# Performance work log

Measured on AMD Instinct MI355X. Metric: run time of the kernel, lower is better.

## Reference

```python
import jax, jax.numpy as jnp
import numpy as np

H = 256
NUM_HEADS = 4
HEAD_DIM = H // NUM_HEADS


def _mlp(x, W1, b1, W2, b2):
    # Linear(2H->H) + ReLU + (dropout=identity in eval) + Linear(H->H)
    h = jax.nn.relu(x @ W1.T + b1)
    return h @ W2.T + b2


def setup_inputs() -> dict:
    key = jax.random.key(0)
    ks = jax.random.split(key, 24)
    s2h = 1.0 / np.sqrt(2 * H)
    sh = 1.0 / np.sqrt(H)
    inp = {
        'qubit_embeddings': jax.random.normal(ks[0], (65536, H), jnp.float32),
        'qpu_embeddings': jax.random.normal(ks[1], (64, H), jnp.float32),
        'gate_embeddings': jax.random.normal(ks[2], (65536, H), jnp.float32),
        'all_embeddings': jax.random.normal(ks[3], (131072, H), jnp.float32),
        'time_table': jax.random.normal(ks[4], (1000, H), jnp.float32),
        'map_W1': jax.random.normal(ks[5], (H, 2 * H), jnp.float32) * s2h,
        'map_b1': jnp.zeros((H,), jnp.float32),
        'map_W2': jax.random.normal(ks[6], (H, H), jnp.float32) * sh,
        'map_b2': jnp.zeros((H,), jnp.float32),
        'sch_W1': jax.random.normal(ks[7], (H, 2 * H), jnp.float32) * s2h,
        'sch_b1': jnp.zeros((H,), jnp.float32),
        'sch_W2': jax.random.normal(ks[8], (H, H), jnp.float32) * sh,
        'sch_b2': jnp.zeros((H,), jnp.float32),
        'qg_W1': jax.random.normal(ks[9], (H, H), jnp.float32) * sh,
        'qg_b1': jnp.zeros((H,), jnp.float32),
        'qg_W2': jax.random.normal(ks[10], (H, H), jnp.float32) * sh,
        'qg_b2': jnp.zeros((H,), jnp.float32),
        'attn_Wq': jax.random.normal(ks[11], (H, H), jnp.float32) * sh,
        'attn_bq': jnp.zeros((H,), jnp.float32),
        'attn_Wk': jax.random.normal(ks[12], (H, H), jnp.float32) * sh,
        'attn_bk': jnp.zeros((H,), jnp.float32),
        'attn_Wv': jax.random.normal(ks[13], (H, H), jnp.float32) * sh,
        'attn_bv': jnp.zeros((H,), jnp.float32),
        'attn_Wo': jax.random.normal(ks[14], (H, H), jnp.float32) * sh,
        'attn_bo': jnp.zeros((H,), jnp.float32),
        'map_qubit': jax.random.randint(ks[15], (131072,), 0, 65536, jnp.int32),
        'map_qpu': jax.random.randint(ks[16], (131072,), 0, 64, jnp.int32),
        'sched_gate': jax.random.randint(ks[17], (131072,), 0, 65536, jnp.int32),
        'sched_time': jax.random.randint(ks[18], (131072,), 0, 1000, jnp.int32),
    }
    return inp


def reference(qubit_embeddings, qpu_embeddings, gate_embeddings, all_embeddings,
              time_table, map_W1, map_b1, map_W2, map_b2,
              sch_W1, sch_b1, sch_W2, sch_b2,
              qg_W1, qg_b1, qg_W2, qg_b2,
              attn_Wq, attn_bq, attn_Wk, attn_bk, attn_Wv, attn_bv,
              attn_Wo, attn_bo,
              map_qubit, map_qpu, sched_gate, sched_time):
    # Vectorized form of the per-action Python loop: gather + concat + MLP.
    map_in = jnp.concatenate([qubit_embeddings[map_qubit], qpu_embeddings[map_qpu]], axis=-1)  # [Nm, 2H]
    map_keys = _mlp(map_in, map_W1, map_b1, map_W2, map_b2)                                    # [Nm, H]
    sch_in = jnp.concatenate([gate_embeddings[sched_gate], time_table[sched_time]], axis=-1)   # [Ns, 2H]
    sch_keys = _mlp(sch_in, sch_W1, sch_b1, sch_W2, sch_b2)                                    # [Ns, H]
    keys = jnp.concatenate([map_keys, sch_keys], axis=0)                                       # [A, H]

    g = all_embeddings.mean(axis=0)                                                            # [H]
    query = jax.nn.relu(g @ qg_W1.T + qg_b1) @ qg_W2.T + qg_b2                                 # [H]

    # MultiheadAttention: batch=1, q_len=1, kv_len=A (dropout=0 in eval, mask all-valid).
    q = (query @ attn_Wq.T + attn_bq).reshape(NUM_HEADS, HEAD_DIM)
    k = (keys @ attn_Wk.T + attn_bk).reshape(-1, NUM_HEADS, HEAD_DIM)
    v = (keys @ attn_Wv.T + attn_bv).reshape(-1, NUM_HEADS, HEAD_DIM)
    scores = jnp.einsum('hd,ahd->ha', q, k) / jnp.sqrt(jnp.asarray(HEAD_DIM, q.dtype))
    w = jax.nn.softmax(scores, axis=-1)                                                        # [heads, A]
    ctx = jnp.einsum('ha,ahd->hd', w, v).reshape(H)
    attn_out = ctx @ attn_Wo.T + attn_bo                                                       # [H]

    action_logits = keys @ attn_out                                                            # [A]
    action_probs = jax.nn.softmax(action_logits, axis=-1)
    return action_probs, action_logits
```

## Files before the change

kernel.cpp:

```cpp
#include <hip/hip_runtime.h>
#include <cstdint>
#include <cstddef>

typedef __bf16 bf16_t;
typedef __bf16 bf16x8 __attribute__((ext_vector_type(8)));
typedef __bf16 bf16x4 __attribute__((ext_vector_type(4)));
typedef float f32x4 __attribute__((ext_vector_type(4)));

#define A_TOTAL 262144
#define NMAP    131072

__global__ __launch_bounds__(256) void k_w1b16(
    const float* __restrict__ mW1, const float* __restrict__ sW1,
    bf16_t* __restrict__ dst) {
  int e = blockIdx.x * 256 + threadIdx.x;
  int slice = e >> 16, idx = e & 65535;
  int n = idx >> 8, k = idx & 255;
  float v;
  switch (slice) {
    case 0:  v = mW1[n * 512 + k]; break;
    case 1:  v = mW1[n * 512 + 256 + k]; break;
    case 2:  v = sW1[n * 512 + k]; break;
    default: v = sW1[n * 512 + 256 + k]; break;
  }
  dst[e] = (bf16_t)v;
}

__global__ __launch_bounds__(256) void k_mean(const float* __restrict__ A,
                                              float* __restrict__ part) {
  int t = threadIdx.x, b = blockIdx.x;
  const float* base = A + (size_t)b * 512 * 256 + t;
  float s = 0.f;
  for (int r = 0; r < 512; ++r) s += base[(size_t)r * 256];
  part[b * 256 + t] = s;
}

__global__ __launch_bounds__(256) void k_front(
    const float* __restrict__ meanPart,
    const float* __restrict__ qgW1, const float* __restrict__ qgb1,
    const float* __restrict__ qgW2, const float* __restrict__ qgb2,
    const float* __restrict__ Wq,  const float* __restrict__ bq,
    const float* __restrict__ Wk,
    const float* __restrict__ mW2, const float* __restrict__ sW2,
    float* __restrict__ qw) {
  __shared__ float g[256], h1[256], qry[256], qv[256];
  __shared__ float qks[4][256];
  int t = threadIdx.x;
  float s = 0.f;
  for (int b = 0; b < 256; ++b) s += meanPart[b * 256 + t];
  g[t] = s * (1.0f / 131072.0f);
  __syncthreads();
  {
    const f32x4* row = (const f32x4*)(qgW1 + (size_t)t * 256);
    float acc = 0.f;
    for (int k = 0; k < 64; ++k) {
      f32x4 w = row[k];
      acc += w[0] * g[4 * k] + w[1] * g[4 * k + 1] + w[2] * g[4 * k + 2] + w[3] * g[4 * k + 3];
    }
    h1[t] = fmaxf(acc + qgb1[t], 0.f);
  }
  __syncthreads();
  {
    const f32x4* row = (const f32x4*)(qgW2 + (size_t)t * 256);
    float acc = 0.f;
    for (int k = 0; k < 64; ++k) {
      f32x4 w = row[k];
      acc += w[0] * h1[4 * k] + w[1] * h1[4 * k + 1] + w[2] * h1[4 * k + 2] + w[3] * h1[4 * k + 3];
    }
    qry[t] = acc + qgb2[t];
  }
  __syncthreads();
  {
    const f32x4* row = (const f32x4*)(Wq + (size_t)t * 256);
    float acc = 0.f;
    for (int k = 0; k < 64; ++k) {
      f32x4 w = row[k];
      acc += w[0] * qry[4 * k] + w[1] * qry[4 * k + 1] + w[2] * qry[4 * k + 2] + w[3] * qry[4 * k + 3];
    }
    qv[t] = acc + bq[t];
  }
  __syncthreads();
  for (int h = 0; h < 4; ++h) {
    float acc = 0.f;
    for (int d = 0; d < 64; ++d) acc += qv[h * 64 + d] * Wk[(size_t)(h * 64 + d) * 256 + t];
    qks[h][t] = acc * 0.125f;
  }
  __syncthreads();
  for (int tab = 0; tab < 2; ++tab) {
    const float* W2 = tab ? sW2 : mW2;
    float acc0 = 0.f, acc1 = 0.f, acc2 = 0.f, acc3 = 0.f;
    for (int n = 0; n < 256; ++n) {
      float wv = W2[(size_t)n * 256 + t];
      acc0 += qks[0][n] * wv;
      acc1 += qks[1][n] * wv;
      acc2 += qks[2][n] * wv;
      acc3 += qks[3][n] * wv;
    }
    float* dst = qw + tab * 1024;
    dst[0 * 256 + t] = acc0;
    dst[1 * 256 + t] = acc1;
    dst[2 * 256 + t] = acc2;
    dst[3 * 256 + t] = acc3;
  }
}

__global__ __launch_bounds__(512, 4) void gemm_direct3(
    const float* __restrict__ A0, int M0, const bf16_t* __restrict__ W0,
    const float* __restrict__ b0, bf16_t* __restrict__ C0, int split,
    const float* __restrict__ A1, int M1, const bf16_t* __restrict__ W1,
    const float* __restrict__ b1, bf16_t* __restrict__ C1) {
  __shared__ __align__(16) bf16_t Xo[128][264];
  int blk = blockIdx.x;
  const float* A; int M; const bf16_t* W; const float* bias; bf16_t* C; int bid;
  if (blk < split) { A = A0; M = M0; W = W0; bias = b0; C = C0; bid = blk; }
  else             { A = A1; M = M1; W = W1; bias = b1; C = C1; bid = blk - split; }
  int t = threadIdx.x;
  int w = t >> 6, lane = t & 63;
  int lm = lane & 15, q = lane >> 4;
  int mloc0 = (w & 1) * 64;
  int m0 = bid * 128 + mloc0;
  int c0 = (w >> 1) * 64;
  int rows[4];
#pragma unroll
  for (int i = 0; i < 4; ++i) {
    int m = m0 + i * 16 + lm;
    rows[i] = m < M ? m : M - 1;
  }
  f32x4 acc[4][4] = {};
#pragma unroll
  for (int kt = 0; kt < 8; ++kt) {
    int k0 = kt * 32 + q * 8;
    bf16x8 b[4];
#pragma unroll
    for (int j = 0; j < 4; ++j)
      b[j] = *(const bf16x8*)(W + (size_t)(c0 + j * 16 + lm) * 256 + k0);
#pragma unroll
    for (int i = 0; i < 4; ++i) {
      const float* src = A + (size_t)rows[i] * 256 + k0;
      f32x4 lo = *(const f32x4*)src;
      f32x4 hi = *(const f32x4*)(src + 4);
      bf16x8 a;
#pragma unroll
      for (int x = 0; x < 4; ++x) { a[x] = (bf16_t)lo[x]; a[x + 4] = (bf16_t)hi[x]; }
#pragma unroll
      for (int j = 0; j < 4; ++j)
        acc[i][j] = __builtin_amdgcn_mfma_f32_16x16x32_bf16(a, b[j], acc[i][j], 0, 0, 0);
    }
  }
#pragma unroll
  for (int j = 0; j < 4; ++j) {
    int col = c0 + j * 16 + lm;
    float bb = bias ? bias[col] : 0.f;
#pragma unroll
    for (int i = 0; i < 4; ++i)
#pragma unroll
      for (int r = 0; r < 4; ++r)
        Xo[mloc0 + i * 16 + q * 4 + r][col] = (bf16_t)(acc[i][j][r] + bb);
  }
  __syncthreads();
  size_t tile0 = (size_t)bid * 128;
  const char* lds = (const char*)&Xo[0][0];
#pragma unroll
  for (int s = 0; s < 8; ++s) {
    int flat = s * 8192 + t * 16;
    int row = flat >> 9, colb = flat & 511;
    if (tile0 + (size_t)row < (size_t)M) {
      uint4 v = *(const uint4*)(lds + row * 528 + colb);
      *(uint4*)((char*)C + tile0 * 512 + (size_t)flat) = v;
    }
  }
}

__global__ __launch_bounds__(256) void k_gx(
    const bf16_t* __restrict__ Pa0, const bf16_t* __restrict__ Pb0,
    const int* __restrict__ idxA0, const int* __restrict__ idxB0,
    const bf16_t* __restrict__ Pa1, const bf16_t* __restrict__ Pb1,
    const int* __restrict__ idxA1, const int* __restrict__ idxB1,
    const float* __restrict__ qw,
    bf16_t* __restrict__ X, float* __restrict__ scores,
    float* __restrict__ partMax) {
  __shared__ float qs[4][256];
  __shared__ float sc[4][64];
  int t = threadIdx.x;
  int b = blockIdx.x;
  int rows0 = b * 64;
  int half = rows0 >= NMAP ? 1 : 0;
  const bf16_t* Pa = half ? Pa1 : Pa0;
  const bf16_t* Pb = half ? Pb1 : Pb0;
  const int* idxA = half ? idxA1 : idxA0;
  const int* idxB = half ? idxB1 : idxB0;
  int lrow0 = rows0 - half * NMAP;

  {
    f32x4 v = *(const f32x4*)(qw + half * 1024 + t * 4);
    *(f32x4*)&((float*)qs)[t * 4] = v;
  }

  int rg = t >> 5;
  int cl = t & 31;
  int ia[8], ib[8];
#pragma unroll
  for (int it = 0; it < 8; ++it) {
    ia[it] = idxA[lrow0 + it * 8 + rg];
    ib[it] = idxB[lrow0 + it * 8 + rg];
  }
  __syncthreads();

#pragma unroll
  for (int it = 0; it < 8; ++it) {
    int rowg = it * 8 + rg;
    bf16x8 a8 = *(const bf16x8*)(Pa + (size_t)ia[it] * 256 + cl * 8);
    bf16x8 b8 = *(const bf16x8*)(Pb + (size_t)ib[it] * 256 + cl * 8);
    float x[8];
    bf16x8 xo;
#pragma unroll
    for (int e = 0; e < 8; ++e) {
      x[e] = fmaxf((float)a8[e] + (float)b8[e], 0.f);
      xo[e] = (bf16_t)x[e];
    }
    *(bf16x8*)(X + (size_t)(rows0 + rowg) * 256 + cl * 8) = xo;
    float p[4] = {0.f, 0.f, 0.f, 0.f};
#pragma unroll
    for (int h = 0; h < 4; ++h)
#pragma unroll
      for (int e = 0; e < 8; ++e)
        p[h] += x[e] * qs[h][cl * 8 + e];
#pragma unroll
    for (int h = 0; h < 4; ++h) {
#pragma unroll
      for (int o = 16; o > 0; o >>= 1) p[h] += __shfl_xor(p[h], o);
      if (cl == 0) sc[h][rowg] = p[h];
    }
  }
  __syncthreads();
  {
    int h = t >> 6, l = t & 63;
    float v = sc[h][l];
    scores[(size_t)h * A_TOTAL + rows0 + l] = v;
    float m = v;
#pragma unroll
    for (int o = 32; o > 0; o >>= 1) m = fmaxf(m, __shfl_xor(m, o));
    if (l == 0) partMax[h * 4096 + b] = m;
  }
}

__global__ __launch_bounds__(256) void k_smax2(const float* __restrict__ pM,
                                               float* __restrict__ Mh) {
  int t = threadIdx.x;
  __shared__ float red[256];
  for (int h = 0; h < 4; ++h) {
    float m = -3.4e38f;
    for (int i = t; i < 4096; i += 256) m = fmaxf(m, pM[h * 4096 + i]);
    red[t] = m;
    __syncthreads();
    for (int s = 128; s > 0; s >>= 1) {
      if (t < s) red[t] = fmaxf(red[t], red[t + s]);
      __syncthreads();
    }
    if (t == 0) Mh[h] = red[0];
    __syncthreads();
  }
}

__global__ __launch_bounds__(256) void k_ssum(const float* __restrict__ scores,
                                              const float* __restrict__ Mh,
                                              float* __restrict__ part) {
  int b = blockIdx.x, t = threadIdx.x;
  float m = Mh[b >> 6];
  const float* base = scores + (size_t)b * 4096;
  float s = 0.f;
  for (int i = 0; i < 16; ++i) s += __expf(base[i * 256 + t] - m);
  __shared__ float red[256];
  red[t] = s;
  __syncthreads();
  for (int st = 128; st > 0; st >>= 1) {
    if (t < st) red[t] += red[t + st];
    __syncthreads();
  }
  if (t == 0) part[b] = red[0];
}

__global__ __launch_bounds__(256) void k_ssum2(const float* __restrict__ part,
                                               float* __restrict__ invS) {
  int t = threadIdx.x;
  __shared__ float red[256];
  red[t] = part[t];
  __syncthreads();
  for (int s = 32; s > 0; s >>= 1) {
    if ((t & 63) < s) red[t] += red[t + s];
    __syncthreads();
  }
  if ((t & 63) == 0) invS[t >> 6] = 1.0f / red[t];
}

__global__ __launch_bounds__(256) void k_u3(
    const bf16_t* __restrict__ X, const float* __restrict__ scores,
    const float* __restrict__ Mh, const float* __restrict__ invS,
    float* __restrict__ y, float* __restrict__ shalf) {
  __shared__ float wl[4][512];
  __shared__ float uloc[8][4][256];
  int t = threadIdx.x;
  int a0 = blockIdx.x * 512;
  int half = blockIdx.x >> 8;
#pragma unroll
  for (int i = 0; i < 8; ++i) {
    int e = i * 256 + t;
    int h = e >> 9, rr = e & 511;
    wl[h][rr] = __expf(scores[(size_t)h * A_TOTAL + a0 + rr] - Mh[h]) * invS[h];
  }
  __syncthreads();
  {
    int h = t >> 6, l = t & 63;
    float s = 0.f;
#pragma unroll
    for (int j = 0; j < 8; ++j) s += wl[h][l + j * 64];
#pragma unroll
    for (int o = 32; o > 0; o >>= 1) s += __shfl_xor(s, o);
    if (l == 0) atomicAdd(&shalf[half * 4 + h], s);
  }
  int tc = t & 31, rh = t >> 5;
  float acc[4][8] = {};
  for (int rr = 0; rr < 64; ++rr) {
    int al = rh * 64 + rr;
    bf16x8 kv = *(const bf16x8*)(X + (size_t)(a0 + al) * 256 + tc * 8);
    float f[8];
#pragma unroll
    for (int e = 0; e < 8; ++e) f[e] = (float)kv[e];
#pragma unroll
    for (int h = 0; h < 4; ++h) {
      float wv = wl[h][al];
#pragma unroll
      for (int e = 0; e < 8; ++e) acc[h][e] += wv * f[e];
    }
  }
#pragma unroll
  for (int h = 0; h < 4; ++h)
#pragma unroll
    for (int e = 0; e < 8; ++e) uloc[rh][h][tc * 8 + e] = acc[h][e];
  __syncthreads();
#pragma unroll
  for (int h = 0; h < 4; ++h) {
    float v = 0.f;
#pragma unroll
    for (int g = 0; g < 8; ++g) v += uloc[g][h][t];
    atomicAdd(&y[(half * 4 + h) * 256 + t], v);
  }
}

__global__ __launch_bounds__(256) void k_attn2(
    const float* __restrict__ y,
    const float* __restrict__ shalf,
    const float* __restrict__ mW2, const float* __restrict__ sW2,
    const float* __restrict__ mb2, const float* __restrict__ sb2,
    const float* __restrict__ Wv, const float* __restrict__ bv,
    const float* __restrict__ Wo, const float* __restrict__ bo,
    float* __restrict__ attnv, float* __restrict__ c01) {
  __shared__ float ys[2][4][256];
  __shared__ float us[4][256];
  __shared__ float ctx[256];
  __shared__ float att[256];
  __shared__ float r0[4], r1[4];
  int t = threadIdx.x;
#pragma unroll
  for (int i = 0; i < 8; ++i) ((float*)ys)[i * 256 + t] = y[i * 256 + t];
  __syncthreads();
  {
    int j = t;
    float a0 = 0.f, a1 = 0.f, a2 = 0.f, a3 = 0.f;
    const f32x4* rm = (const f32x4*)(mW2 + (size_t)j * 256);
    const f32x4* rs = (const f32x4*)(sW2 + (size_t)j * 256);
    for (int k = 0; k < 64; ++k) {
      f32x4 wm = rm[k], wsv = rs[k];
#pragma unroll
      for (int e = 0; e < 4; ++e) {
        float w0 = wm[e], w1 = wsv[e];
        int kk = k * 4 + e;
        a0 += ys[0][0][kk] * w0 + ys[1][0][kk] * w1;
        a1 += ys[0][1][kk] * w0 + ys[1][1][kk] * w1;
        a2 += ys[0][2][kk] * w0 + ys[1][2][kk] * w1;
        a3 += ys[0][3][kk] * w0 + ys[1][3][kk] * w1;
      }
    }
    float bm = mb2[j], bs = sb2[j];
    us[0][j] = a0 + shalf[0] * bm + shalf[4] * bs;
    us[1][j] = a1 + shalf[1] * bm + shalf[5] * bs;
    us[2][j] = a2 + shalf[2] * bm + shalf[6] * bs;
    us[3][j] = a3 + shalf[3] * bm + shalf[7] * bs;
  }
  __syncthreads();
  {
    int h = t >> 6;
    const f32x4* row = (const f32x4*)(Wv + (size_t)t * 256);
    const f32x4* uh = (const f32x4*)us[h];
    float acc = 0.f;
    for (int k = 0; k < 64; ++k) {
      f32x4 w = row[k], x = uh[k];
      acc += w[0] * x[0] + w[1] * x[1] + w[2] * x[2] + w[3] * x[3];
    }
    ctx[t] = acc + bv[t];
  }
  __syncthreads();
  {
    const f32x4* row = (const f32x4*)(Wo + (size_t)t * 256);
    const f32x4* cx = (const f32x4*)ctx;
    float acc = 0.f;
    for (int k = 0; k < 64; ++k) {
      f32x4 w = row[k], x = cx[k];
      acc += w[0] * x[0] + w[1] * x[1] + w[2] * x[2] + w[3] * x[3];
    }
    float v = acc + bo[t];
    att[t] = v;
    attnv[t] = v;
  }
  __syncthreads();
  {
    float p0 = mb2[t] * att[t], p1 = sb2[t] * att[t];
#pragma unroll
    for (int o = 32; o > 0; o >>= 1) {
      p0 += __shfl_xor(p0, o);
      p1 += __shfl_xor(p1, o);
    }
    if ((t & 63) == 0) { r0[t >> 6] = p0; r1[t >> 6] = p1; }
    __syncthreads();
    if (t == 0) c01[0] = r0[0] + r0[1] + r0[2] + r0[3];
    if (t == 1) c01[1] = r1[0] + r1[1] + r1[2] + r1[3];
  }
}

__global__ __launch_bounds__(256) void k_zc(
    const float* __restrict__ mW2, const float* __restrict__ sW2,
    const float* __restrict__ attnv, bf16_t* __restrict__ zpad) {
  int tab = blockIdx.x, t = threadIdx.x;
  const float* W2 = tab ? sW2 : mW2;
  __shared__ float att[256];
  att[t] = attnv[t];
  __syncthreads();
  float acc = 0.f;
  for (int j = 0; j < 256; ++j) acc += W2[(size_t)j * 256 + t] * att[j];
  bf16_t* dst = zpad + (size_t)tab * 16 * 256;
  dst[t] = (bf16_t)acc;
#pragma unroll
  for (int i = 1; i < 16; ++i) dst[i * 256 + t] = (bf16_t)0.f;
}

__global__ __launch_bounds__(256) void k_logits3(
    const bf16_t* __restrict__ X, const bf16_t* __restrict__ zpad,
    const float* __restrict__ c01,
    float* __restrict__ out_logits, float* __restrict__ blockMax) {
  int t = threadIdx.x;
  int w = t >> 6, lane = t & 63;
  int lm = lane & 15, q = lane >> 4;
  int half = blockIdx.x >> 9;
  float c = c01[half];
  int m0 = blockIdx.x * 256 + w * 64;
  const bf16_t* zp = zpad + (size_t)half * 16 * 256;
  bf16x8 b[8];
#pragma unroll
  for (int kt = 0; kt < 8; ++kt)
    b[kt] = *(const bf16x8*)(zp + lm * 256 + kt * 32 + q * 8);
  f32x4 acc[4] = {};
#pragma unroll
  for (int i = 0; i < 4; ++i) {
    const bf16_t* arow = X + (size_t)(m0 + i * 16 + lm) * 256 + q * 8;
#pragma unroll
    for (int kt = 0; kt < 8; ++kt) {
      bf16x8 a = *(const bf16x8*)(arow + kt * 32);
      acc[i] = __builtin_amdgcn_mfma_f32_16x16x32_bf16(a, b[kt], acc[i], 0, 0, 0);
    }
  }
  float lmax = -3.4e38f;
  if (lm == 0) {
#pragma unroll
    for (int i = 0; i < 4; ++i) {
      f32x4 v4;
#pragma unroll
      for (int rr = 0; rr < 4; ++rr) {
        float v = acc[i][rr] + c;
        v4[rr] = v;
        lmax = fmaxf(lmax, v);
      }
      *(f32x4*)(out_logits + m0 + i * 16 + q * 4) = v4;
    }
  }
  float m1 = fmaxf(lmax, __shfl_xor(lmax, 16));
  float m2 = fmaxf(m1, __shfl_xor(m1, 32));
  __shared__ float red[4];
  if (lane == 0) red[w] = m2;
  __syncthreads();
  if (t == 0)
    blockMax[blockIdx.x] = fmaxf(fmaxf(red[0], red[1]), fmaxf(red[2], red[3]));
}

__global__ __launch_bounds__(256) void k_lred1(const float* __restrict__ bm,
                                               float* __restrict__ Ml) {
  int t = threadIdx.x;
  float m = -3.4e38f;
  for (int i = t; i < 1024; i += 256) m = fmaxf(m, bm[i]);
  __shared__ float red[256];
  red[t] = m;
  __syncthreads();
  for (int s = 128; s > 0; s >>= 1) {
    if (t < s) red[t] = fmaxf(red[t], red[t + s]);
    __syncthreads();
  }
  if (t == 0) Ml[0] = red[0];
}

__global__ __launch_bounds__(256) void k_lsum(const float* __restrict__ logits,
                                              const float* __restrict__ Ml,
                                              float* __restrict__ part) {
  int t = threadIdx.x, b = blockIdx.x;
  float m = Ml[0];
  float s = __expf(logits[b * 512 + t] - m) + __expf(logits[b * 512 + 256 + t] - m);
  __shared__ float red[256];
  red[t] = s;
  __syncthreads();
  for (int st = 128; st > 0; st >>= 1) {
    if (t < st) red[t] += red[t + st];
    __syncthreads();
  }
  if (t == 0) part[b] = red[0];
}

__global__ __launch_bounds__(256) void k_lred2(const float* __restrict__ part,
                                               float* __restrict__ invSl) {
  int t = threadIdx.x;
  float s = part[t] + part[t + 256];
  __shared__ float red[256];
  red[t] = s;
  __syncthreads();
  for (int st = 128; st > 0; st >>= 1) {
    if (t < st) red[t] += red[t + st];
    __syncthreads();
  }
  if (t == 0) invSl[0] = 1.0f / red[0];
}

__global__ __launch_bounds__(256) void k_probs(const float* __restrict__ logits,
                                               const float* __restrict__ Ml,
                                               const float* __restrict__ invSl,
                                               float* __restrict__ probs) {
  int i = blockIdx.x * 256 + threadIdx.x;
  probs[i] = __expf(logits[i] - Ml[0]) * invSl[0];
}

extern "C" void kernel_launch(void* const* d_in, const int* in_sizes, int n_in,
                              void* d_out, int out_size, void* d_ws, size_t ws_size,
                              hipStream_t stream) {
  const float* qubit_emb = (const float*)d_in[0];
  const float* qpu_emb   = (const float*)d_in[1];
  const float* gate_emb  = (const float*)d_in[2];
  const float* all_emb   = (const float*)d_in[3];
  const float* time_tab  = (const float*)d_in[4];
  const float* map_W1 = (const float*)d_in[5];
  const float* map_b1 = (const float*)d_in[6];
  const float* map_W2 = (const float*)d_in[7];
  const float* map_b2 = (const float*)d_in[8];
  const float* sch_W1 = (const float*)d_in[9];
  const float* sch_b1 = (const float*)d_in[10];
  const float* sch_W2 = (const float*)d_in[11];
  const float* sch_b2 = (const float*)d_in[12];
  const float* qg_W1 = (const float*)d_in[13];
  const float* qg_b1 = (const float*)d_in[14];
  const float* qg_W2 = (const float*)d_in[15];
  const float* qg_b2 = (const float*)d_in[16];
  const float* Wq = (const float*)d_in[17];
  const float* bq = (const float*)d_in[18];
  const float* Wk = (const float*)d_in[19];
  const float* Wv = (const float*)d_in[21];
  const float* bv = (const float*)d_in[22];
  const float* Wo = (const float*)d_in[23];
  const float* bo = (const float*)d_in[24];
  const int* map_qubit  = (const int*)d_in[25];
  const int* map_qpu    = (const int*)d_in[26];
  const int* sched_gate = (const int*)d_in[27];
  const int* sched_time = (const int*)d_in[28];
  (void)in_sizes; (void)n_in; (void)out_size;

  char* ws = (char*)d_ws;
  size_t off = 0;
  auto alloc = [&](size_t b) { size_t r = off; off += (b + 255) & ~(size_t)255; return r; };
  size_t XB    = alloc((size_t)A_TOTAL * 256 * 2);
  size_t PQ    = alloc((size_t)65536 * 256 * 2);
  size_t PG    = alloc((size_t)65536 * 256 * 2);
  size_t PP    = alloc((size_t)128 * 256 * 2);
  size_t PT    = alloc((size_t)1024 * 256 * 2);
  size_t W1B   = alloc((size_t)4 * 65536 * 2);
  size_t QW    = alloc((size_t)2 * 4 * 256 * 4);
  size_t SCORE = alloc((size_t)4 * A_TOTAL * 4);
  size_t MPART = alloc((size_t)256 * 256 * 4);
  size_t ZPAD  = alloc((size_t)2 * 16 * 256 * 2);
  size_t ATTNV = alloc(256 * 4);
  size_t Y     = alloc(2 * 4 * 256 * 4);
  size_t SH    = alloc(2 * 4 * 4);
  size_t C01   = alloc(2 * 4);
  size_t PMAX  = alloc(4 * 4096 * 4);
  size_t MH    = alloc(4 * 4);
  size_t SINV  = alloc(4 * 4);
  size_t BMAX  = alloc(1024 * 4);
  size_t ML    = alloc(4);
  size_t SLINV = alloc(4);
  size_t LPART = alloc(512 * 4);
  size_t SPART = alloc(256 * 4);
  if (off > ws_size) return;

  bf16_t* xP     = (bf16_t*)(ws + XB);
  bf16_t* pqP    = (bf16_t*)(ws + PQ);
  bf16_t* pgP    = (bf16_t*)(ws + PG);
  bf16_t* ppP    = (bf16_t*)(ws + PP);
  bf16_t* ptP    = (bf16_t*)(ws + PT);
  bf16_t* w1bP   = (bf16_t*)(ws + W1B);
  float*  qwP    = (float*)(ws + QW);
  float*  scoreP = (float*)(ws + SCORE);
  float*  mpartP = (float*)(ws + MPART);
  bf16_t* zpadP  = (bf16_t*)(ws + ZPAD);
  float*  attnvP = (float*)(ws + ATTNV);
  float*  yP     = (float*)(ws + Y);
  float*  shP    = (float*)(ws + SH);
  float*  c01P   = (float*)(ws + C01);
  float*  pmaxP  = (float*)(ws + PMAX);
  float*  mhP    = (float*)(ws + MH);
  float*  sinvP  = (float*)(ws + SINV);
  float*  bmaxP  = (float*)(ws + BMAX);
  float*  mlP    = (float*)(ws + ML);
  float*  slinvP = (float*)(ws + SLINV);
  float*  lpartP = (float*)(ws + LPART);
  float*  spartP = (float*)(ws + SPART);

  float* probsOut  = (float*)d_out;
  float* logitsOut = probsOut + A_TOTAL;

  hipMemsetAsync(yP, 0, 8448, stream);

  k_w1b16<<<1024, 256, 0, stream>>>(map_W1, sch_W1, w1bP);
  k_mean<<<256, 256, 0, stream>>>(all_emb, mpartP);
  k_front<<<1, 256, 0, stream>>>(mpartP, qg_W1, qg_b1, qg_W2, qg_b2,
                                 Wq, bq, Wk, map_W2, sch_W2, qwP);

  gemm_direct3<<<1024, 512, 0, stream>>>(
      qubit_emb, 65536, w1bP + 0 * 65536, nullptr, pqP, 512,
      gate_emb,  65536, w1bP + 2 * 65536, nullptr, pgP);
  gemm_direct3<<<9, 512, 0, stream>>>(
      qpu_emb, 64,   w1bP + 1 * 65536, map_b1, ppP, 1,
      time_tab, 1000, w1bP + 3 * 65536, sch_b1, ptP);

  k_gx<<<4096, 256, 0, stream>>>(
      pqP, ppP, map_qubit, map_qpu,
      pgP, ptP, sched_gate, sched_time,
      qwP, xP, scoreP, pmaxP);

  k_smax2<<<1, 256, 0, stream>>>(pmaxP, mhP);
  k_ssum<<<256, 256, 0, stream>>>(scoreP, mhP, spartP);
  k_ssum2<<<1, 256, 0, stream>>>(spartP, sinvP);

  k_u3<<<512, 256, 0, stream>>>(xP, scoreP, mhP, sinvP, yP, shP);
  k_attn2<<<1, 256, 0, stream>>>(yP, shP, map_W2, sch_W2, map_b2, sch_b2,
                                 Wv, bv, Wo, bo, attnvP, c01P);
  k_zc<<<2, 256, 0, stream>>>(map_W2, sch_W2, attnvP, zpadP);

  k_logits3<<<1024, 256, 0, stream>>>(xP, zpadP, c01P, logitsOut, bmaxP);
  k_lred1<<<1, 256, 0, stream>>>(bmaxP, mlP);
  k_lsum<<<512, 256, 0, stream>>>(logitsOut, mlP, lpartP);
  k_lred2<<<1, 256, 0, stream>>>(lpartP, slinvP);
  k_probs<<<1024, 256, 0, stream>>>(logitsOut, mlP, slinvP, probsOut);
}
```

Before: 717.1 us.

## Fuse softmax reductions via last-block pattern and parallelize tail matvecs

Online max/sum partials are now computed inside k_gx and k_logits4. A last-block atomic counter does the final reduction there, which removes several small reduction kernels and one re-read of the scores and logits arrays. The single-block attention tail (k_attn2, k_zc) is split into multi-block matvec kernels, and c01 is accumulated with atomics. k_mean is vectorised to f32x4 loads, and the GEMM epilogue LDS buffer is halved to allow higher occupancy. The memset is extended to cover the counters and c01, and atomic float accumulation changes summation order.

Result: slower. 1.597 ms (+122.7%).

```diff
diff --git a/kernel.cpp b/kernel.cpp
--- a/kernel.cpp
+++ b/kernel.cpp
@@ -28,11 +28,20 @@
 
 __global__ __launch_bounds__(256) void k_mean(const float* __restrict__ A,
                                               float* __restrict__ part) {
+  __shared__ f32x4 sred[4][64];
   int t = threadIdx.x, b = blockIdx.x;
-  const float* base = A + (size_t)b * 512 * 256 + t;
-  float s = 0.f;
-  for (int r = 0; r < 512; ++r) s += base[(size_t)r * 256];
-  part[b * 256 + t] = s;
+  int cg = t & 63, rs = t >> 6;
+  const float* base = A + ((size_t)b * 512 + rs * 128) * 256 + cg * 4;
+  f32x4 acc = {};
+#pragma unroll 4
+  for (int r = 0; r < 128; ++r)
+    acc += *(const f32x4*)(base + (size_t)r * 256);
+  sred[rs][cg] = acc;
+  __syncthreads();
+  if (t < 64) {
+    f32x4 tot = sred[0][t] + sred[1][t] + sred[2][t] + sred[3][t];
+    *(f32x4*)(part + b * 256 + t * 4) = tot;
+  }
 }
 
 __global__ __launch_bounds__(256) void k_front(
@@ -104,12 +113,12 @@
   }
 }
 
-__global__ __launch_bounds__(512, 4) void gemm_direct3(
+__global__ __launch_bounds__(512, 8) void gemm_direct4(
     const float* __restrict__ A0, int M0, const bf16_t* __restrict__ W0,
     const float* __restrict__ b0, bf16_t* __restrict__ C0, int split,
     const float* __restrict__ A1, int M1, const bf16_t* __restrict__ W1,
     const float* __restrict__ b1, bf16_t* __restrict__ C1) {
-  __shared__ __align__(16) bf16_t Xo[128][264];
+  __shared__ __align__(16) bf16_t Xo[64][264];
   int blk = blockIdx.x;
   const float* A; int M; const bf16_t* W; const float* bias; bf16_t* C; int bid;
   if (blk < split) { A = A0; M = M0; W = W0; bias = b0; C = C0; bid = blk; }
@@ -117,8 +126,7 @@
   int t = threadIdx.x;
   int w = t >> 6, lane = t & 63;
   int lm = lane & 15, q = lane >> 4;
-  int mloc0 = (w & 1) * 64;
-  int m0 = bid * 128 + mloc0;
+  int m0 = bid * 128 + (w & 1) * 64;
   int c0 = (w >> 1) * 64;
   int rows[4];
 #pragma unroll
@@ -148,25 +156,31 @@
     }
   }
 #pragma unroll
-  for (int j = 0; j < 4; ++j) {
-    int col = c0 + j * 16 + lm;
-    float bb = bias ? bias[col] : 0.f;
-#pragma unroll
-    for (int i = 0; i < 4; ++i)
-#pragma unroll
-      for (int r = 0; r < 4; ++r)
-        Xo[mloc0 + i * 16 + q * 4 + r][col] = (bf16_t)(acc[i][j][r] + bb);
-  }
-  __syncthreads();
-  size_t tile0 = (size_t)bid * 128;
-  const char* lds = (const char*)&Xo[0][0];
-#pragma unroll
-  for (int s = 0; s < 8; ++s) {
-    int flat = s * 8192 + t * 16;
-    int row = flat >> 9, colb = flat & 511;
-    if (tile0 + (size_t)row < (size_t)M) {
-      uint4 v = *(const uint4*)(lds + row * 528 + colb);
-      *(uint4*)((char*)C + tile0 * 512 + (size_t)flat) = v;
+  for (int p = 0; p < 2; ++p) {
+    if (p) __syncthreads();
+    if ((w & 1) == p) {
+#pragma unroll
+      for (int j = 0; j < 4; ++j) {
+        int col = c0 + j * 16 + lm;
+        float bb = bias ? bias[col] : 0.f;
+#pragma unroll
+        for (int i = 0; i < 4; ++i)
+#pragma unroll
+          for (int r = 0; r < 4; ++r)
+            Xo[i * 16 + q * 4 + r][col] = (bf16_t)(acc[i][j][r] + bb);
+      }
+    }
+    __syncthreads();
+    size_t tile0 = (size_t)bid * 128 + p * 64;
+    const char* lds = (const char*)&Xo[0][0];
+#pragma unroll
+    for (int s = 0; s < 4; ++s) {
+      int flat = s * 8192 + t * 16;
+      int row = flat >> 9, colb = flat & 511;
+      if (tile0 + (size_t)row < (size_t)M) {
+        uint4 v = *(const uint4*)(lds + row * 528 + colb);
+        *(uint4*)((char*)C + tile0 * 512 + (size_t)flat) = v;
+      }
     }
   }
 }
@@ -178,9 +192,12 @@
     const int* __restrict__ idxA1, const int* __restrict__ idxB1,
     const float* __restrict__ qw,
     bf16_t* __restrict__ X, float* __restrict__ scores,
-    float* __restrict__ partMax) {
+    float* __restrict__ partMax, float* __restrict__ partSum,
+    int* __restrict__ cnt, float* __restrict__ Mh, float* __restrict__ sinv) {
   __shared__ float qs[4][256];
   __shared__ float sc[4][64];
+  __shared__ float redM[256], redS[256];
+  __shared__ int isLast;
   int t = threadIdx.x;
   int b = blockIdx.x;
   int rows0 = b * 64;
@@ -240,57 +257,42 @@
     float m = v;
 #pragma unroll
     for (int o = 32; o > 0; o >>= 1) m = fmaxf(m, __shfl_xor(m, o));
-    if (l == 0) partMax[h * 4096 + b] = m;
-  }
-}
-
-__global__ __launch_bounds__(256) void k_smax2(const float* __restrict__ pM,
-                                               float* __restrict__ Mh) {
-  int t = threadIdx.x;
-  __shared__ float red[256];
+    float s = __expf(v - m);
+#pragma unroll
+    for (int o = 32; o > 0; o >>= 1) s += __shfl_xor(s, o);
+    if (l == 0) {
+      partMax[h * 4096 + b] = m;
+      partSum[h * 4096 + b] = s;
+    }
+  }
+  __threadfence();
+  __syncthreads();
+  if (t == 0) isLast = (atomicAdd(cnt, 1) == (int)gridDim.x - 1);
+  __syncthreads();
+  if (!isLast) return;
+  __threadfence();
   for (int h = 0; h < 4; ++h) {
-    float m = -3.4e38f;
-    for (int i = t; i < 4096; i += 256) m = fmaxf(m, pM[h * 4096 + i]);
-    red[t] = m;
+    float m = -3.4e38f, s = 0.f;
+    for (int i = t; i < 4096; i += 256) {
+      float pm = partMax[h * 4096 + i], ps = partSum[h * 4096 + i];
+      float nm = fmaxf(m, pm);
+      s = s * __expf(m - nm) + ps * __expf(pm - nm);
+      m = nm;
+    }
+    redM[t] = m; redS[t] = s;
     __syncthreads();
-    for (int s = 128; s > 0; s >>= 1) {
-      if (t < s) red[t] = fmaxf(red[t], red[t + s]);
+    for (int st = 128; st > 0; st >>= 1) {
+      if (t < st) {
+        float m2 = redM[t + st], s2 = redS[t + st];
+        float nm = fmaxf(redM[t], m2);
+        redS[t] = redS[t] * __expf(redM[t] - nm) + s2 * __expf(m2 - nm);
+        redM[t] = nm;
+      }
       __syncthreads();
     }
-    if (t == 0) Mh[h] = red[0];
+    if (t == 0) { Mh[h] = redM[0]; sinv[h] = 1.0f / redS[0]; }
     __syncthreads();
   }
-}
-
-__global__ __launch_bounds__(256) void k_ssum(const float* __restrict__ scores,
-                                              const float* __restrict__ Mh,
-                                              float* __restrict__ part) {
-  int b = blockIdx.x, t = threadIdx.x;
-  float m = Mh[b >> 6];
-  const float* base = scores + (size_t)b * 4096;
-  float s = 0.f;
-  for (int i = 0; i < 16; ++i) s += __expf(base[i * 256 + t] - m);
-  __shared__ float red[256];
-  red[t] = s;
-  __syncthreads();
-  for (int st = 128; st > 0; st >>= 1) {
-    if (t < st) red[t] += red[t + st];
-    __syncthreads();
-  }
-  if (t == 0) part[b] = red[0];
-}
-
-__global__ __launch_bounds__(256) void k_ssum2(const float* __restrict__ part,
-                                               float* __restrict__ invS) {
-  int t = threadIdx.x;
-  __shared__ float red[256];
-  red[t] = part[t];
-  __syncthreads();
-  for (int s = 32; s > 0; s >>= 1) {
-    if ((t & 63) < s) red[t] += red[t + s];
-    __syncthreads();
-  }
-  if ((t & 63) == 0) invS[t >> 6] = 1.0f / red[t];
 }
 
 __global__ __launch_bounds__(256) void k_u3(
@@ -347,106 +349,110 @@
   }
 }
 
-__global__ __launch_bounds__(256) void k_attn2(
-    const float* __restrict__ y,
-    const float* __restrict__ shalf,
+__global__ __launch_bounds__(256) void k_u4(
+    const float* __restrict__ y, const float* __restrict__ shalf,
     const float* __restrict__ mW2, const float* __restrict__ sW2,
     const float* __restrict__ mb2, const float* __restrict__ sb2,
-    const float* __restrict__ Wv, const float* __restrict__ bv,
-    const float* __restrict__ Wo, const float* __restrict__ bo,
-    float* __restrict__ attnv, float* __restrict__ c01) {
-  __shared__ float ys[2][4][256];
-  __shared__ float us[4][256];
-  __shared__ float ctx[256];
-  __shared__ float att[256];
-  __shared__ float r0[4], r1[4];
+    float* __restrict__ u) {
+  __shared__ float wsum[4][4];
+  int j = blockIdx.x, t = threadIdx.x;
+  int w = t >> 6, lane = t & 63;
+  float pm = mW2[(size_t)j * 256 + t], ps = sW2[(size_t)j * 256 + t];
+  float p[4];
+#pragma unroll
+  for (int h = 0; h < 4; ++h)
+    p[h] = y[(0 + h) * 256 + t] * pm + y[(4 + h) * 256 + t] * ps;
+#pragma unroll
+  for (int h = 0; h < 4; ++h)
+#pragma unroll
+    for (int o = 32; o > 0; o >>= 1) p[h] += __shfl_xor(p[h], o);
+  if (lane == 0)
+#pragma unroll
+    for (int h = 0; h < 4; ++h) wsum[w][h] = p[h];
+  __syncthreads();
+  if (t < 4) {
+    float tot = wsum[0][t] + wsum[1][t] + wsum[2][t] + wsum[3][t];
+    u[t * 256 + j] = tot + shalf[t] * mb2[j] + shalf[4 + t] * sb2[j];
+  }
+}
+
+__global__ __launch_bounds__(256) void k_ctx(
+    const float* __restrict__ u, const float* __restrict__ Wv,
+    const float* __restrict__ bv, float* __restrict__ ctxv) {
+  __shared__ float wsum[4];
+  int j = blockIdx.x, t = threadIdx.x;
+  int w = t >> 6, lane = t & 63;
+  int h = j >> 6;
+  float p = Wv[(size_t)j * 256 + t] * u[h * 256 + t];
+#pragma unroll
+  for (int o = 32; o > 0; o >>= 1) p += __shfl_xor(p, o);
+  if (lane == 0) wsum[w] = p;
+  __syncthreads();
+  if (t == 0)
+    ctxv[j] = wsum[0] + wsum[1] + wsum[2] + wsum[3] + bv[j];
+}
+
+__global__ __launch_bounds__(256) void k_att(
+    const float* __restrict__ ctxv, const float* __restrict__ Wo,
+    const float* __restrict__ bo,
+    const float* __restrict__ mb2, const float* __restrict__ sb2,
+    float* __restrict__ attv, float* __restrict__ c01) {
+  __shared__ float wsum[4];
+  int j = blockIdx.x, t = threadIdx.x;
+  int w = t >> 6, lane = t & 63;
+  float p = Wo[(size_t)j * 256 + t] * ctxv[t];
+#pragma unroll
+  for (int o = 32; o > 0; o >>= 1) p += __shfl_xor(p, o);
+  if (lane == 0) wsum[w] = p;
+  __syncthreads();
+  if (t == 0) {
+    float a = wsum[0] + wsum[1] + wsum[2] + wsum[3] + bo[j];
+    attv[j] = a;
+    atomicAdd(&c01[0], mb2[j] * a);
+    atomicAdd(&c01[1], sb2[j] * a);
+  }
+}
+
+__global__ __launch_bounds__(256) void k_z(
+    const float* __restrict__ mW2, const float* __restrict__ sW2,
+    const float* __restrict__ attv, float* __restrict__ zpart) {
+  __shared__ float as[16];
+  int b = blockIdx.x, t = threadIdx.x;
+  int tab = b >> 4, jc = b & 15;
+  const float* W2 = tab ? sW2 : mW2;
+  if (t < 16) as[t] = attv[jc * 16 + t];
+  __syncthreads();
+  float acc = 0.f;
+#pragma unroll
+  for (int i = 0; i < 16; ++i)
+    acc += as[i] * W2[(size_t)(jc * 16 + i) * 256 + t];
+  zpart[b * 256 + t] = acc;
+}
+
+__global__ __launch_bounds__(256) void k_zfin(
+    const float* __restrict__ zpart, bf16_t* __restrict__ zpad) {
   int t = threadIdx.x;
 #pragma unroll
-  for (int i = 0; i < 8; ++i) ((float*)ys)[i * 256 + t] = y[i * 256 + t];
-  __syncthreads();
-  {
-    int j = t;
-    float a0 = 0.f, a1 = 0.f, a2 = 0.f, a3 = 0.f;
-    const f32x4* rm = (const f32x4*)(mW2 + (size_t)j * 256);
-    const f32x4* rs = (const f32x4*)(sW2 + (size_t)j * 256);
-    for (int k = 0; k < 64; ++k) {
-      f32x4 wm = rm[k], wsv = rs[k];
-#pragma unroll
-      for (int e = 0; e < 4; ++e) {
-        float w0 = wm[e], w1 = wsv[e];
-        int kk = k * 4 + e;
-        a0 += ys[0][0][kk] * w0 + ys[1][0][kk] * w1;
-        a1 += ys[0][1][kk] * w0 + ys[1][1][kk] * w1;
-        a2 += ys[0][2][kk] * w0 + ys[1][2][kk] * w1;
-        a3 += ys[0][3][kk] * w0 + ys[1][3][kk] * w1;
-      }
-    }
-    float bm = mb2[j], bs = sb2[j];
-    us[0][j] = a0 + shalf[0] * bm + shalf[4] * bs;
-    us[1][j] = a1 + shalf[1] * bm + shalf[5] * bs;
-    us[2][j] = a2 + shalf[2] * bm + shalf[6] * bs;
-    us[3][j] = a3 + shalf[3] * bm + shalf[7] * bs;
-  }
-  __syncthreads();
-  {
-    int h = t >> 6;
-    const f32x4* row = (const f32x4*)(Wv + (size_t)t * 256);
-    const f32x4* uh = (const f32x4*)us[h];
-    float acc = 0.f;
-    for (int k = 0; k < 64; ++k) {
-      f32x4 w = row[k], x = uh[k];
-      acc += w[0] * x[0] + w[1] * x[1] + w[2] * x[2] + w[3] * x[3];
-    }
-    ctx[t] = acc + bv[t];
-  }
-  __syncthreads();
-  {
-    const f32x4* row = (const f32x4*)(Wo + (size_t)t * 256);
-    const f32x4* cx = (const f32x4*)ctx;
-    float acc = 0.f;
-    for (int k = 0; k < 64; ++k) {
-      f32x4 w = row[k], x = cx[k];
-      acc += w[0] * x[0] + w[1] * x[1] + w[2] * x[2] + w[3] * x[3];
-    }
-    float v = acc + bo[t];
-    att[t] = v;
-    attnv[t] = v;
-  }
-  __syncthreads();
-  {
-    float p0 = mb2[t] * att[t], p1 = sb2[t] * att[t];
-#pragma unroll
-    for (int o = 32; o > 0; o >>= 1) {
-      p0 += __shfl_xor(p0, o);
-      p1 += __shfl_xor(p1, o);
-    }
-    if ((t & 63) == 0) { r0[t >> 6] = p0; r1[t >> 6] = p1; }
-    __syncthreads();
-    if (t == 0) c01[0] = r0[0] + r0[1] + r0[2] + r0[3];
-    if (t == 1) c01[1] = r1[0] + r1[1] + r1[2] + r1[3];
-  }
-}
-
-__global__ __launch_bounds__(256) void k_zc(
-    const float* __restrict__ mW2, const float* __restrict__ sW2,
-    const float* __restrict__ attnv, bf16_t* __restrict__ zpad) {
-  int tab = blockIdx.x, t = threadIdx.x;
-  const float* W2 = tab ? sW2 : mW2;
-  __shared__ float att[256];
-  att[t] = attnv[t];
-  __syncthreads();
-  float acc = 0.f;
-  for (int j = 0; j < 256; ++j) acc += W2[(size_t)j * 256 + t] * att[j];
-  bf16_t* dst = zpad + (size_t)tab * 16 * 256;
-  dst[t] = (bf16_t)acc;
-#pragma unroll
-  for (int i = 1; i < 16; ++i) dst[i * 256 + t] = (bf16_t)0.f;
-}
-
-__global__ __launch_bounds__(256) void k_logits3(
+  for (int tab = 0; tab < 2; ++tab) {
+    float s = 0.f;
+#pragma unroll
+    for (int i = 0; i < 16; ++i) s += zpart[(tab * 16 + i) * 256 + t];
+    bf16_t* dst = zpad + (size_t)tab * 16 * 256;
+    dst[t] = (bf16_t)s;
+#pragma unroll
+    for (int i = 1; i < 16; ++i) dst[i * 256 + t] = (bf16_t)0.f;
+  }
+}
+
+__global__ __launch_bounds__(256) void k_logits4(
     const bf16_t* __restrict__ X, const bf16_t* __restrict__ zpad,
     const float* __restrict__ c01,
-    float* __restrict__ out_logits, float* __restrict__ blockMax) {
+    float* __restrict__ out_logits,
+    float* __restrict__ blockMax, float* __restrict__ blockSum,
+    int* __restrict__ cnt, float* __restrict__ Ml, float* __restrict__ invSl) {
+  __shared__ float redm[4], reds[4];
+  __shared__ float redM[256], redS[256];
+  __shared__ int isLast;
   int t = threadIdx.x;
   int w = t >> 6, lane = t & 63;
   int lm = lane & 15, q = lane >> 4;
@@ -468,6 +474,7 @@
       acc[i] = __builtin_amdgcn_mfma_f32_16x16x32_bf16(a, b[kt], acc[i], 0, 0, 0);
     }
   }
+  float vals[16];
   float lmax = -3.4e38f;
   if (lm == 0) {
 #pragma unroll
@@ -476,6 +483,7 @@
 #pragma unroll
       for (int rr = 0; rr < 4; ++rr) {
         float v = acc[i][rr] + c;
+        vals[i * 4 + rr] = v;
         v4[rr] = v;
         lmax = fmaxf(lmax, v);
       }
@@ -484,56 +492,47 @@
   }
   float m1 = fmaxf(lmax, __shfl_xor(lmax, 16));
   float m2 = fmaxf(m1, __shfl_xor(m1, 32));
-  __shared__ float red[4];
-  if (lane == 0) red[w] = m2;
-  __syncthreads();
-  if (t == 0)
-    blockMax[blockIdx.x] = fmaxf(fmaxf(red[0], red[1]), fmaxf(red[2], red[3]));
-}
-
-__global__ __launch_bounds__(256) void k_lred1(const float* __restrict__ bm,
-                                               float* __restrict__ Ml) {
-  int t = threadIdx.x;
-  float m = -3.4e38f;
-  for (int i = t; i < 1024; i += 256) m = fmaxf(m, bm[i]);
-  __shared__ float red[256];
-  red[t] = m;
-  __syncthreads();
-  for (int s = 128; s > 0; s >>= 1) {
-    if (t < s) red[t] = fmaxf(red[t], red[t + s]);
+  if (lane == 0) redm[w] = m2;
+  __syncthreads();
+  float mb = fmaxf(fmaxf(redm[0], redm[1]), fmaxf(redm[2], redm[3]));
+  float s = 0.f;
+  if (lm == 0) {
+#pragma unroll
+    for (int i2 = 0; i2 < 16; ++i2) s += __expf(vals[i2] - mb);
+  }
+  s += __shfl_xor(s, 16);
+  s += __shfl_xor(s, 32);
+  if (lane == 0) reds[w] = s;
+  __syncthreads();
+  if (t == 0) {
+    blockMax[blockIdx.x] = mb;
+    blockSum[blockIdx.x] = reds[0] + reds[1] + reds[2] + reds[3];
+  }
+  __threadfence();
+  __syncthreads();
+  if (t == 0) isLast = (atomicAdd(cnt, 1) == (int)gridDim.x - 1);
+  __syncthreads();
+  if (!isLast) return;
+  __threadfence();
+  float m = -3.4e38f, ssum = 0.f;
+  for (int i = t; i < 1024; i += 256) {
+    float pm = blockMax[i], ps = blockSum[i];
+    float nm = fmaxf(m, pm);
+    ssum = ssum * __expf(m - nm) + ps * __expf(pm - nm);
+    m = nm;
+  }
+  redM[t] = m; redS[t] = ssum;
+  __syncthreads();
+  for (int st = 128; st > 0; st >>= 1) {
+    if (t < st) {
+      float mo = redM[t + st], so = redS[t + st];
+      float nm = fmaxf(redM[t], mo);
+      redS[t] = redS[t] * __expf(redM[t] - nm) + so * __expf(mo - nm);
+      redM[t] = nm;
+    }
     __syncthreads();
   }
-  if (t == 0) Ml[0] = red[0];
-}
-
-__global__ __launch_bounds__(256) void k_lsum(const float* __restrict__ logits,
-                                              const float* __restrict__ Ml,
-                                              float* __restrict__ part) {
-  int t = threadIdx.x, b = blockIdx.x;
-  float m = Ml[0];
-  float s = __expf(logits[b * 512 + t] - m) + __expf(logits[b * 512 + 256 + t] - m);
-  __shared__ float red[256];
-  red[t] = s;
-  __syncthreads();
-  for (int st = 128; st > 0; st >>= 1) {
-    if (t < st) red[t] += red[t + st];
-    __syncthreads();
-  }
-  if (t == 0) part[b] = red[0];
-}
-
-__global__ __launch_bounds__(256) void k_lred2(const float* __restrict__ part,
-                                               float* __restrict__ invSl) {
-  int t = threadIdx.x;
-  float s = part[t] + part[t + 256];
-  __shared__ float red[256];
-  red[t] = s;
-  __syncthreads();
-  for (int st = 128; st > 0; st >>= 1) {
-    if (t < st) red[t] += red[t + st];
-    __syncthreads();
-  }
-  if (t == 0) invSl[0] = 1.0f / red[0];
+  if (t == 0) { Ml[0] = redM[0]; invSl[0] = 1.0f / redS[0]; }
 }
 
 __global__ __launch_bounds__(256) void k_probs(const float* __restrict__ logits,
@@ -590,18 +589,22 @@
   size_t SCORE = alloc((size_t)4 * A_TOTAL * 4);
   size_t MPART = alloc((size_t)256 * 256 * 4);
   size_t ZPAD  = alloc((size_t)2 * 16 * 256 * 2);
-  size_t ATTNV = alloc(256 * 4);
+  size_t ZPART = alloc((size_t)32 * 256 * 4);
+  size_t U     = alloc(4 * 256 * 4);
+  size_t CTXV  = alloc(256 * 4);
+  size_t ATTV  = alloc(256 * 4);
   size_t Y     = alloc(2 * 4 * 256 * 4);
   size_t SH    = alloc(2 * 4 * 4);
   size_t C01   = alloc(2 * 4);
+  size_t CNT   = alloc(2 * 4);
   size_t PMAX  = alloc(4 * 4096 * 4);
+  size_t PSUM  = alloc(4 * 4096 * 4);
   size_t MH    = alloc(4 * 4);
   size_t SINV  = alloc(4 * 4);
   size_t BMAX  = alloc(1024 * 4);
+  size_t BSUM  = alloc(1024 * 4);
   size_t ML    = alloc(4);
   size_t SLINV = alloc(4);
-  size_t LPART = alloc(512 * 4);
-  size_t SPART = alloc(256 * 4);
   if (off > ws_size) return;
 
   bf16_t* xP     = (bf16_t*)(ws + XB);
@@ -614,53 +617,53 @@
   float*  scoreP = (float*)(ws + SCORE);
   float*  mpartP = (float*)(ws + MPART);
   bf16_t* zpadP  = (bf16_t*)(ws + ZPAD);
-  float*  attnvP = (float*)(ws + ATTNV);
+  float*  zpartP = (float*)(ws + ZPART);
+  float*  uP     = (float*)(ws + U);
+  float*  ctxvP  = (float*)(ws + CTXV);
+  float*  attvP  = (float*)(ws + ATTV);
   float*  yP     = (float*)(ws + Y);
   float*  shP    = (float*)(ws + SH);
   float*  c01P   = (float*)(ws + C01);
+  int*    cntP   = (int*)(ws + CNT);
   float*  pmaxP  = (float*)(ws + PMAX);
+  float*  psumP  = (float*)(ws + PSUM);
   float*  mhP    = (float*)(ws + MH);
   float*  sinvP  = (float*)(ws + SINV);
   float*  bmaxP  = (float*)(ws + BMAX);
+  float*  bsumP  = (float*)(ws + BSUM);
   float*  mlP    = (float*)(ws + ML);
   float*  slinvP = (float*)(ws + SLINV);
-  float*  lpartP = (float*)(ws + LPART);
-  float*  spartP = (float*)(ws + SPART);
 
   float* probsOut  = (float*)d_out;
   float* logitsOut = probsOut + A_TOTAL;
 
-  hipMemsetAsync(yP, 0, 8448, stream);
+  hipMemsetAsync(yP, 0, 8960, stream);
 
   k_w1b16<<<1024, 256, 0, stream>>>(map_W1, sch_W1, w1bP);
   k_mean<<<256, 256, 0, stream>>>(all_emb, mpartP);
   k_front<<<1, 256, 0, stream>>>(mpartP, qg_W1, qg_b1, qg_W2, qg_b2,
                                  Wq, bq, Wk, map_W2, sch_W2, qwP);
 
-  gemm_direct3<<<1024, 512, 0, stream>>>(
+  gemm_direct4<<<1024, 512, 0, stream>>>(
       qubit_emb, 65536, w1bP + 0 * 65536, nullptr, pqP, 512,
       gate_emb,  65536, w1bP + 2 * 65536, nullptr, pgP);
-  gemm_direct3<<<9, 512, 0, stream>>>(
+  gemm_direct4<<<9, 512, 0, stream>>>(
       qpu_emb, 64,   w1bP + 1 * 65536, map_b1, ppP, 1,
       time_tab, 1000, w1bP + 3 * 65536, sch_b1, ptP);
 
   k_gx<<<4096, 256, 0, stream>>>(
       pqP, ppP, map_qubit, map_qpu,
       pgP, ptP, sched_gate, sched_time,
-      qwP, xP, scoreP, pmaxP);
-
-  k_smax2<<<1, 256, 0, stream>>>(pmaxP, mhP);
-  k_ssum<<<256, 256, 0, stream>>>(scoreP, mhP, spartP);
-  k_ssum2<<<1, 256, 0, stream>>>(spartP, sinvP);
+      qwP, xP, scoreP, pmaxP, psumP, cntP + 0, mhP, sinvP);
 
   k_u3<<<512, 256, 0, stream>>>(xP, scoreP, mhP, sinvP, yP, shP);
-  k_attn2<<<1, 256, 0, stream>>>(yP, shP, map_W2, sch_W2, map_b2, sch_b2,
-                                 Wv, bv, Wo, bo, attnvP, c01P);
-  k_zc<<<2, 256, 0, stream>>>(map_W2, sch_W2, attnvP, zpadP);
-
-  k_logits3<<<1024, 256, 0, stream>>>(xP, zpadP, c01P, logitsOut, bmaxP);
-  k_lred1<<<1, 256, 0, stream>>>(bmaxP, mlP);
-  k_lsum<<<512, 256, 0, stream>>>(logitsOut, mlP, lpartP);
-  k_lred2<<<1, 256, 0, stream>>>(lpartP, slinvP);
+  k_u4<<<256, 256, 0, stream>>>(yP, shP, map_W2, sch_W2, map_b2, sch_b2, uP);
+  k_ctx<<<256, 256, 0, stream>>>(uP, Wv, bv, ctxvP);
+  k_att<<<256, 256, 0, stream>>>(ctxvP, Wo, bo, map_b2, sch_b2, attvP, c01P);
+  k_z<<<32, 256, 0, stream>>>(map_W2, sch_W2, attvP, zpartP);
+  k_zfin<<<1, 256, 0, stream>>>(zpartP, zpadP);
+
+  k_logits4<<<1024, 256, 0, stream>>>(xP, zpadP, c01P, logitsOut,
+                                      bmaxP, bsumP, cntP + 1, mlP, slinvP);
   k_probs<<<1024, 256, 0, stream>>>(logitsOut, mlP, slinvP, probsOut);
 }
```
